# Kernel optimization log

Hardware: AMD Instinct MI355X
Metric: run time of the kernel (lower is better)

Reference implementation:

```python
import jax, jax.numpy as jnp
import numpy as np

K = 3        # cubic spline degree (hardcoded in module: self.k = 3)
N_KNOTS = 5  # n_knots


def _deboor_np(x, t, c, k):
    """Vectorized de Boor evaluation in numpy (used only to build the
    collocation matrix replicating scipy.splrep interpolation)."""
    m = np.clip(np.searchsorted(t, x, side='right') - 1, k, len(t) - k - 2)
    d = [c[m - k + j] for j in range(k + 1)]
    for r in range(1, k + 1):
        for j in range(k, r - 1, -1):
            left = t[j + m - k]
            right = t[j + 1 + m - r]
            denom = right - left
            safe = np.where(denom > 0, denom, 1.0)
            alpha = np.where(denom > 0, (x - left) / safe, 0.0)
            d[j] = (1.0 - alpha) * d[j - 1] + alpha * d[j]
    return d[k]


def setup_inputs() -> dict:
    key = jax.random.key(0)
    rng = np.random.default_rng(0)
    x_kn = np.linspace(0.0, 1.0, N_KNOTS)
    y_kn = rng.random(N_KNOTS)
    y_kn[0] = 0.0
    y_kn[-1] = 1.0
    # FITPACK interpolation knot layout for n=5, k=3: clamped ends + interior knot at x[2]
    t = np.concatenate([np.zeros(K + 1), x_kn[2:-2], np.ones(K + 1)]).astype(np.float64)
    # collocation matrix A[j, i] = B_i(x_j); solve A c = y  (splrep with s=0)
    eye = np.eye(N_KNOTS)
    A = np.stack([_deboor_np(x_kn, t, eye[i], K) for i in range(N_KNOTS)], axis=1)
    c = np.linalg.solve(A, y_kn)
    imgs = jax.random.uniform(key, (64, 3, 512, 512), dtype=jnp.float32)
    return {
        "imgs": imgs,
        "t": jnp.asarray(t, dtype=jnp.float32),
        "c": jnp.asarray(c, dtype=jnp.float32),
    }


def reference(imgs, t, c):
    """Elementwise cubic B-spline evaluation of imgs via de Boor's recursion,
    then zero-masking where the input was exactly zero (as in the torch module)."""
    k = K
    # interval index: t[m] <= x < t[m+1], clamped so boundary/extrapolation
    # uses the edge polynomial (matches scipy BSpline extrapolate=True)
    m = jnp.clip(jnp.searchsorted(t, imgs, side='right') - 1, k, t.shape[0] - k - 2)
    d = [c[m - k + j] for j in range(k + 1)]  # k+1 local coefficients per pixel
    for r in range(1, k + 1):
        for j in range(k, r - 1, -1):
            left = t[j + m - k]
            right = t[j + 1 + m - r]
            denom = right - left
            safe = jnp.where(denom > 0, denom, 1.0)
            alpha = jnp.where(denom > 0, (imgs - left) / safe, 0.0)
            d[j] = (1.0 - alpha) * d[j - 1] + alpha * d[j]
    out = d[k]
    return jnp.where(imgs == 0, jnp.zeros((), dtype=out.dtype), out)
```

## Files before the change

kernel.cpp:

```cpp
#include <hip/hip_runtime.h>


__global__ __launch_bounds__(256) void bspline_kernel(
    const float4* __restrict__ in4,
    float4* __restrict__ out4,
    const float* __restrict__ t,
    const float* __restrict__ c,
    int n4)
{
    const float t1 = t[1], t2 = t[2], t3 = t[3], t4 = t[4],
                t5 = t[5], t6 = t[6], t7 = t[7];
    const float c0 = c[0], c1 = c[1], c2 = c[2], c3 = c[3], c4 = c[4];

    auto rdf = [](float lo, float hi) -> float {
        float d = hi - lo;
        return d > 0.f ? 1.f / d : 0.f;
    };

    const float L13_3 = t3, L13_4 = t4, RD13_3 = rdf(t3, t6), RD13_4 = rdf(t4, t7);
    const float L12_3 = t2, L12_4 = t3, RD12_3 = rdf(t2, t5), RD12_4 = rdf(t3, t6);
    const float L11_3 = t1, L11_4 = t2, RD11_3 = rdf(t1, t4), RD11_4 = rdf(t2, t5);
    const float L23_3 = t3, L23_4 = t4, RD23_3 = rdf(t3, t5), RD23_4 = rdf(t4, t6);
    const float L22_3 = t2, L22_4 = t3, RD22_3 = rdf(t2, t4), RD22_4 = rdf(t3, t5);
    const float L33_3 = t3, L33_4 = t4, RD33_3 = rdf(t3, t4), RD33_4 = rdf(t4, t5);

    auto eval = [&](float x) -> float {
        const bool up = (x >= t4);
        float d0 = up ? c1 : c0;
        float d1 = up ? c2 : c1;
        float d2 = up ? c3 : c2;
        float d3 = up ? c4 : c3;
        float a;
        a = (x - (up ? L13_4 : L13_3)) * (up ? RD13_4 : RD13_3);
        d3 = fmaf(a, d3 - d2, d2);
        a = (x - (up ? L12_4 : L12_3)) * (up ? RD12_4 : RD12_3);
        d2 = fmaf(a, d2 - d1, d1);
        a = (x - (up ? L11_4 : L11_3)) * (up ? RD11_4 : RD11_3);
        d1 = fmaf(a, d1 - d0, d0);
        a = (x - (up ? L23_4 : L23_3)) * (up ? RD23_4 : RD23_3);
        d3 = fmaf(a, d3 - d2, d2);
        a = (x - (up ? L22_4 : L22_3)) * (up ? RD22_4 : RD22_3);
        d2 = fmaf(a, d2 - d1, d1);
        a = (x - (up ? L33_4 : L33_3)) * (up ? RD33_4 : RD33_3);
        d3 = fmaf(a, d3 - d2, d2);
        return (x == 0.f) ? 0.f : d3;
    };

    const int stride = gridDim.x * blockDim.x;
    for (int i = blockIdx.x * blockDim.x + threadIdx.x; i < n4; i += stride) {
        float4 v = in4[i];
        float4 o;
        o.x = eval(v.x);
        o.y = eval(v.y);
        o.z = eval(v.z);
        o.w = eval(v.w);
        out4[i] = o;
    }
}

extern "C" void kernel_launch(void* const* d_in, const int* in_sizes, int n_in,
                              void* d_out, int out_size, void* d_ws, size_t ws_size,
                              hipStream_t stream) {
    const float* imgs = (const float*)d_in[0];
    const float* t    = (const float*)d_in[1];
    const float* c    = (const float*)d_in[2];
    float* out = (float*)d_out;

    const int n  = in_sizes[0];
    const int n4 = n / 4;

    const int block = 256;
    int grid = 8192;
    int max_grid = (n4 + block - 1) / block;
    if (grid > max_grid) grid = max_grid;

    bspline_kernel<<<grid, block, 0, stream>>>(
        (const float4*)imgs, (float4*)out, t, c, n4);
}
```

Before: 332.1 us.

## Precompute piecewise cubic polynomial coefficients and use nontemporal 2x-unrolled loads

Measured after the change: 319.2 us. 3.9% less time.

```diff
diff --git a/kernel.cpp b/kernel.cpp
--- a/kernel.cpp
+++ b/kernel.cpp
@@ -1,60 +1,90 @@
 #include <hip/hip_runtime.h>
 
 
+typedef float v4f __attribute__((ext_vector_type(4)));
+
+template<int M>
+__device__ inline void expand_piece(const float tt[9], const float cc[5],
+                                    float out[4]) {
+    float P[4][4];
+#pragma unroll
+    for (int j = 0; j < 4; ++j) {
+        P[j][0] = cc[M - 3 + j];
+        P[j][1] = 0.f; P[j][2] = 0.f; P[j][3] = 0.f;
+    }
+#pragma unroll
+    for (int r = 1; r <= 3; ++r) {
+#pragma unroll
+        for (int j = 3; j >= 1; --j) {
+            if (j < r) continue;
+            const float L   = tt[j + M - 3];
+            const float R   = tt[j + 1 + M - r];
+            const float den = R - L;
+            const float rd  = den > 0.f ? 1.f / den : 0.f;
+            const float p = rd;
+            const float q = -rd * L;
+            const float e0 = P[j][0] - P[j-1][0];
+            const float e1 = P[j][1] - P[j-1][1];
+            const float e2 = P[j][2] - P[j-1][2];
+            const float e3 = P[j][3] - P[j-1][3];
+            P[j][0] = P[j-1][0] + q * e0;
+            P[j][1] = P[j-1][1] + q * e1 + p * e0;
+            P[j][2] = P[j-1][2] + q * e2 + p * e1;
+            P[j][3] = P[j-1][3] + q * e3 + p * e2;
+        }
+    }
+#pragma unroll
+    for (int i = 0; i < 4; ++i) out[i] = P[3][i];
+}
+
 __global__ __launch_bounds__(256) void bspline_kernel(
-    const float4* __restrict__ in4,
-    float4* __restrict__ out4,
+    const v4f* __restrict__ in4,
+    v4f* __restrict__ out4,
     const float* __restrict__ t,
     const float* __restrict__ c,
     int n4)
 {
-    const float t1 = t[1], t2 = t[2], t3 = t[3], t4 = t[4],
-                t5 = t[5], t6 = t[6], t7 = t[7];
-    const float c0 = c[0], c1 = c[1], c2 = c[2], c3 = c[3], c4 = c[4];
+    float tt[9], cc[5];
+#pragma unroll
+    for (int i = 0; i < 9; ++i) tt[i] = t[i];
+#pragma unroll
+    for (int i = 0; i < 5; ++i) cc[i] = c[i];
 
-    auto rdf = [](float lo, float hi) -> float {
-        float d = hi - lo;
-        return d > 0.f ? 1.f / d : 0.f;
-    };
-
-    const float L13_3 = t3, L13_4 = t4, RD13_3 = rdf(t3, t6), RD13_4 = rdf(t4, t7);
-    const float L12_3 = t2, L12_4 = t3, RD12_3 = rdf(t2, t5), RD12_4 = rdf(t3, t6);
-    const float L11_3 = t1, L11_4 = t2, RD11_3 = rdf(t1, t4), RD11_4 = rdf(t2, t5);
-    const float L23_3 = t3, L23_4 = t4, RD23_3 = rdf(t3, t5), RD23_4 = rdf(t4, t6);
-    const float L22_3 = t2, L22_4 = t3, RD22_3 = rdf(t2, t4), RD22_4 = rdf(t3, t5);
-    const float L33_3 = t3, L33_4 = t4, RD33_3 = rdf(t3, t4), RD33_4 = rdf(t4, t5);
+    float A[4], B[4];
+    expand_piece<3>(tt, cc, A);
+    expand_piece<4>(tt, cc, B);
+    const float t4 = tt[4];
 
     auto eval = [&](float x) -> float {
         const bool up = (x >= t4);
-        float d0 = up ? c1 : c0;
-        float d1 = up ? c2 : c1;
-        float d2 = up ? c3 : c2;
-        float d3 = up ? c4 : c3;
-        float a;
-        a = (x - (up ? L13_4 : L13_3)) * (up ? RD13_4 : RD13_3);
-        d3 = fmaf(a, d3 - d2, d2);
-        a = (x - (up ? L12_4 : L12_3)) * (up ? RD12_4 : RD12_3);
-        d2 = fmaf(a, d2 - d1, d1);
-        a = (x - (up ? L11_4 : L11_3)) * (up ? RD11_4 : RD11_3);
-        d1 = fmaf(a, d1 - d0, d0);
-        a = (x - (up ? L23_4 : L23_3)) * (up ? RD23_4 : RD23_3);
-        d3 = fmaf(a, d3 - d2, d2);
-        a = (x - (up ? L22_4 : L22_3)) * (up ? RD22_4 : RD22_3);
-        d2 = fmaf(a, d2 - d1, d1);
-        a = (x - (up ? L33_4 : L33_3)) * (up ? RD33_4 : RD33_3);
-        d3 = fmaf(a, d3 - d2, d2);
-        return (x == 0.f) ? 0.f : d3;
+        const float k0 = up ? B[0] : A[0];
+        const float k1 = up ? B[1] : A[1];
+        const float k2 = up ? B[2] : A[2];
+        const float k3 = up ? B[3] : A[3];
+        float y = fmaf(fmaf(fmaf(k3, x, k2), x, k1), x, k0);
+        return (x == 0.f) ? 0.f : y;
     };
 
-    const int stride = gridDim.x * blockDim.x;
-    for (int i = blockIdx.x * blockDim.x + threadIdx.x; i < n4; i += stride) {
-        float4 v = in4[i];
-        float4 o;
-        o.x = eval(v.x);
-        o.y = eval(v.y);
-        o.z = eval(v.z);
-        o.w = eval(v.w);
-        out4[i] = o;
+    const int tid    = blockIdx.x * (blockDim.x * 2) + threadIdx.x;
+    const int stride = gridDim.x * blockDim.x * 2;
+
+    for (int i0 = tid; i0 < n4; i0 += stride) {
+        const int i1 = i0 + blockDim.x;
+        v4f v0 = __builtin_nontemporal_load(&in4[i0]);
+        v4f v1;
+        const bool has1 = (i1 < n4);
+        if (has1) v1 = __builtin_nontemporal_load(&in4[i1]);
+
+        v4f o0, o1;
+        o0.x = eval(v0.x); o0.y = eval(v0.y);
+        o0.z = eval(v0.z); o0.w = eval(v0.w);
+        __builtin_nontemporal_store(o0, &out4[i0]);
+
+        if (has1) {
+            o1.x = eval(v1.x); o1.y = eval(v1.y);
+            o1.z = eval(v1.z); o1.w = eval(v1.w);
+            __builtin_nontemporal_store(o1, &out4[i1]);
+        }
     }
 }
 
@@ -71,9 +101,9 @@
 
     const int block = 256;
     int grid = 8192;
-    int max_grid = (n4 + block - 1) / block;
+    int max_grid = (n4 + block * 2 - 1) / (block * 2);
     if (grid > max_grid) grid = max_grid;
 
     bspline_kernel<<<grid, block, 0, stream>>>(
-        (const float4*)imgs, (float4*)out, t, c, n4);
+        (const v4f*)imgs, (v4f*)out, t, c, n4);
 }
```
